# Optimization experiments

Hardware: AMD Instinct MI355X
Metric: run time of the kernel (lower is better)

Reference implementation:

```python
import jax, jax.numpy as jnp
import numpy as np

B, S, D = 8, 1024, 1024
H, KV, HD = 16, 16, 64
NDIM = 2
EPS = 1e-6


def rms_norm(x, weight=None, eps=EPS):
    var = jnp.mean(jnp.square(x), axis=-1, keepdims=True)
    out = x * jax.lax.rsqrt(var + eps)
    if weight is not None:
        out = out * weight
    return out


def rotate_half(x):
    half = x.shape[-1] // 2
    return jnp.concatenate((-x[..., half:], x[..., :half]), axis=-1)


def multidim_rope(x, cos, sin, ndim):
    # x: [B,S,H,HD]; cos,sin: [B,S,HD]; head_dim split into ndim contiguous
    # chunks of size per = 2*(HD // (2*ndim)); rotate-half applied per chunk.
    b, s, h, hd = x.shape
    per = 2 * (hd // (2 * ndim))
    xg = x.reshape(b, s, h, ndim, per)
    cg = cos.reshape(b, s, 1, ndim, per)
    sg = sin.reshape(b, s, 1, ndim, per)
    out = xg * cg + rotate_half(xg) * sg
    return out.reshape(b, s, h, hd)


def setup_inputs() -> dict:
    key = jax.random.key(0)
    ks = jax.random.split(key, 10)
    scale = 1.0 / np.sqrt(D)
    return {
        "hidden_states": jax.random.normal(ks[0], (B, S, D), jnp.float32),
        "cos": jax.random.uniform(ks[1], (B, S, HD), jnp.float32, -1.0, 1.0),
        "sin": jax.random.uniform(ks[2], (B, S, HD), jnp.float32, -1.0, 1.0),
        "position_ids": jax.random.randint(ks[3], (B, S, NDIM), 0, 32, jnp.int32),
        "wq": jax.random.normal(ks[4], (D, H * HD), jnp.float32) * scale,
        "wk": jax.random.normal(ks[5], (D, KV * HD), jnp.float32) * scale,
        "wv": jax.random.normal(ks[6], (D, KV * HD), jnp.float32) * scale,
        "wo": jax.random.normal(ks[7], (H * HD, D), jnp.float32) * scale,
        "q_norm_w": jnp.ones((HD,), jnp.float32),
        "k_norm_w": jnp.ones((HD,), jnp.float32),
    }


def reference(hidden_states, cos, sin, position_ids, wq, wk, wv, wo, q_norm_w, k_norm_w):
    b, s, _ = hidden_states.shape
    ndim = position_ids.shape[-1]

    q = (hidden_states @ wq).reshape(b, s, H, HD)
    q = rms_norm(q, q_norm_w)
    q = multidim_rope(q, cos, sin, ndim)

    k = (hidden_states @ wk).reshape(b, s, KV, HD)
    k = rms_norm(k, k_norm_w)
    k = multidim_rope(k, cos, sin, ndim)

    v = (hidden_states @ wv).reshape(b, s, KV, HD)
    v = rms_norm(v, None)  # v_norm has no weight

    # Full (non-causal) vision attention, scaling = 1.0
    scores = jnp.einsum("bqhd,bkhd->bhqk", q, k)
    probs = jax.nn.softmax(scores, axis=-1)
    attn = jnp.einsum("bhqk,bkhd->bqhd", probs, v).reshape(b, s, H * HD)

    return attn @ wo
```

## Files before the change

### kernel.cpp

```cpp
#include <hip/hip_runtime.h>
#include <hip/hip_bf16.h>

typedef __attribute__((ext_vector_type(8))) short bf16x8;
typedef __attribute__((ext_vector_type(4))) short bf16x4;
typedef __attribute__((ext_vector_type(4))) float f32x4;

struct __align__(16) V16 { unsigned long long a, b; };

__device__ __forceinline__ float bf2f(unsigned short u) {
  union { unsigned int i; float f; } c; c.i = ((unsigned int)u) << 16; return c.f;
}
__device__ __forceinline__ unsigned short f2bf(float f) {
  unsigned int u; __builtin_memcpy(&u, &f, 4);
  u += 0x7FFFu + ((u >> 16) & 1u);
  return (unsigned short)(u >> 16);
}

__device__ __forceinline__ void async16(unsigned short* lds,
                                        const unsigned short* g) {
  __builtin_amdgcn_global_load_lds(
      (const __attribute__((address_space(1))) unsigned int*)g,
      (__attribute__((address_space(3))) unsigned int*)lds, 16, 0, 0);
}

#define FP32_MAGIC 0x3F800000u

__device__ __forceinline__ void cvt_seg(
    const void* __restrict__ src, unsigned short* __restrict__ dst,
    int n4, int i, int stride, bool f32)
{
  if (f32) {
    const float* s = (const float*)src;
    for (; i < n4; i += stride) {
      float4 v = *(const float4*)(s + (size_t)i * 4);
      ushort2 lo = { f2bf(v.x), f2bf(v.y) };
      ushort2 hi = { f2bf(v.z), f2bf(v.w) };
      *(ushort2*)(dst + (size_t)i * 4)     = lo;
      *(ushort2*)(dst + (size_t)i * 4 + 2) = hi;
    }
  } else {
    const unsigned short* s = (const unsigned short*)src;
    for (; i < n4; i += stride)
      *(ushort4*)(dst + (size_t)i * 4) = *(const ushort4*)(s + (size_t)i * 4);
  }
}

__global__ __launch_bounds__(256) void cvt_bf16(
    const void* __restrict__ src, size_t srcOff,
    unsigned short* __restrict__ dst, int n4,
    const unsigned int* __restrict__ fmt)
{
  const bool f32 = (fmt[0] == FP32_MAGIC);
  const int i = blockIdx.x * blockDim.x + threadIdx.x;
  const int stride = gridDim.x * blockDim.x;
  const void* s = f32 ? (const void*)((const float*)src + srcOff)
                      : (const void*)((const unsigned short*)src + srcOff);
  cvt_seg(s, dst, n4, i, stride, f32);
}

__global__ __launch_bounds__(256) void cvt_all(
    const void* __restrict__ hid, const void* __restrict__ cosr,
    const void* __restrict__ sinr, const void* __restrict__ qnw,
    const void* __restrict__ knw,
    unsigned short* __restrict__ hb, unsigned short* __restrict__ csb,
    unsigned short* __restrict__ snb, unsigned short* __restrict__ qnb,
    unsigned short* __restrict__ knb,
    int hidden_n4, const unsigned int* __restrict__ fmt)
{
  const bool f32 = (fmt[0] == FP32_MAGIC);
  const int bx = blockIdx.x, tid = threadIdx.x;
  if (bx < 2048) {
    if (hidden_n4 > 0)
      cvt_seg(hid, hb, hidden_n4, bx * 256 + tid, 2048 * 256, f32);
  } else if (bx < 2176) {
    cvt_seg(cosr, csb, 131072, (bx - 2048) * 256 + tid, 128 * 256, f32);
  } else if (bx < 2304) {
    cvt_seg(sinr, snb, 131072, (bx - 2176) * 256 + tid, 128 * 256, f32);
  } else {
    if (tid < 16)       cvt_seg(qnw, qnb, 16, tid, 16, f32);
    else if (tid < 32)  cvt_seg(knw, knb, 16, tid - 16, 16, f32);
  }
}

__global__ __launch_bounds__(256) void cvt_t4(
    const void* __restrict__ s0, const void* __restrict__ s1,
    const void* __restrict__ s2, const void* __restrict__ s3,
    unsigned short* __restrict__ d0, unsigned short* __restrict__ d1,
    unsigned short* __restrict__ d2, unsigned short* __restrict__ d3,
    const unsigned int* __restrict__ fmt)
{
  __shared__ __align__(16) unsigned short T[64][72];
  const int z = blockIdx.z;
  const void* src = (z == 0) ? s0 : (z == 1) ? s1 : (z == 2) ? s2 : s3;
  unsigned short* dstT = (z == 0) ? d0 : (z == 1) ? d1 : (z == 2) ? d2 : d3;

  const bool f32 = (fmt[0] == FP32_MAGIC);
  const int tid = threadIdx.x;
  const int k0 = blockIdx.x * 64, n0 = blockIdx.y * 64;
  const int rl = tid >> 3, cl = (tid & 7) * 8;

#pragma unroll
  for (int p = 0; p < 2; ++p) {
    int r = rl + p * 32;
    int cs = cl ^ (r & 56);
    if (f32) {
      const float* s = (const float*)src + (size_t)(k0 + r) * 1024 + n0 + cl;
      float4 v0 = *(const float4*)s, v1 = *(const float4*)(s + 4);
      unsigned short* t = &T[r][cs];
      t[0]=f2bf(v0.x); t[1]=f2bf(v0.y); t[2]=f2bf(v0.z); t[3]=f2bf(v0.w);
      t[4]=f2bf(v1.x); t[5]=f2bf(v1.y); t[6]=f2bf(v1.z); t[7]=f2bf(v1.w);
    } else {
      *(V16*)&T[r][cs] = *(const V16*)((const unsigned short*)src +
                                        (size_t)(k0 + r) * 1024 + n0 + cl);
    }
  }
  __syncthreads();

#pragma unroll
  for (int p = 0; p < 2; ++p) {
    int u = tid + p * 256;
    int d = u >> 3, sc = (u & 7) * 8;
    unsigned short tmp[8];
#pragma unroll
    for (int i = 0; i < 8; ++i) tmp[i] = T[sc + i][d ^ sc];
    *(V16*)&dstT[(size_t)(n0 + d) * 1024 + k0 + sc] = *(V16*)tmp;
  }
}

#define TM 128
#define TN 128
#define TK 64
#define GK 1024

__global__ __launch_bounds__(256) void gemm_qkv(
    const unsigned short* __restrict__ A,
    const unsigned short* __restrict__ Bt,
    unsigned short* __restrict__ Cq,
    unsigned short* __restrict__ Ck,
    unsigned short* __restrict__ Cv,
    const unsigned short* __restrict__ cs,
    const unsigned short* __restrict__ sn,
    const unsigned short* __restrict__ qw,
    const unsigned short* __restrict__ kw,
    int M)
{
  __shared__ __align__(16) unsigned short LDSu[2 * TM * TK];
  unsigned short (*As)[TK] = (unsigned short (*)[TK])LDSu;
  unsigned short (*Bs)[TK] = (unsigned short (*)[TK])&LDSu[TM * TK];

  const int tid  = threadIdx.x;
  const int wave = tid >> 6;
  const int lane = tid & 63;
  const int quad = lane >> 4;
  const int l16  = lane & 15;
  const int bm = blockIdx.x * TM;
  const int bn = blockIdx.y * TN;
  const int wm = (wave & 1) * 64;
  const int wn = (wave >> 1) * 64;

  const f32x4 z = {0.f, 0.f, 0.f, 0.f};
  f32x4 acc[4][4];
#pragma unroll
  for (int i = 0; i < 4; ++i)
#pragma unroll
    for (int j = 0; j < 4; ++j) acc[i][j] = z;

  const int lrow = lane >> 3;
  const int gcol = ((lane & 7) ^ lrow) * 8;
  const unsigned short* aP = A  + (size_t)(bm + wave * 8 + lrow) * GK + gcol;
  const unsigned short* bP = Bt + (size_t)(bn + wave * 8 + lrow) * GK + gcol;
  const int cswz = l16 & 7;

  for (int k0 = 0; k0 < GK; k0 += TK) {
#pragma unroll
    for (int p = 0; p < 4; ++p) {
      async16(&As[p * 32 + wave * 8][0], aP + (size_t)p * 32 * GK);
      async16(&Bs[p * 32 + wave * 8][0], bP + (size_t)p * 32 * GK);
    }
    aP += TK; bP += TK;
    __syncthreads();

#pragma unroll
    for (int s = 0; s < 2; ++s) {
      const int pc = ((s * 4 + quad) ^ cswz) * 8;
      bf16x8 af[4], bfv[4];
#pragma unroll
      for (int mt = 0; mt < 4; ++mt)
        af[mt] = *(const bf16x8*)&As[wm + mt * 16 + l16][pc];
#pragma unroll
      for (int nt = 0; nt < 4; ++nt)
        bfv[nt] = *(const bf16x8*)&Bs[wn + nt * 16 + l16][pc];
#pragma unroll
      for (int mt = 0; mt < 4; ++mt)
#pragma unroll
        for (int nt = 0; nt < 4; ++nt)
          acc[mt][nt] = __builtin_amdgcn_mfma_f32_16x16x32_bf16(
              af[mt], bfv[nt], acc[mt][nt], 0, 0, 0);
    }
    __syncthreads();
  }

  const int which = bn >> 10;
  const int colbase = (bn & 1023) + wn;

  if (which == 2) {
    unsigned short* Tw = LDSu + wave * 4096;
#pragma unroll
    for (int mt = 0; mt < 4; ++mt)
#pragma unroll
      for (int r = 0; r < 4; ++r) {
        const int s = mt * 16 + quad * 4 + r;
        float x0 = acc[mt][0][r], x1 = acc[mt][1][r];
        float x2 = acc[mt][2][r], x3 = acc[mt][3][r];
        float ss = x0 * x0 + x1 * x1 + x2 * x2 + x3 * x3;
        ss += __shfl_xor(ss, 1);
        ss += __shfl_xor(ss, 2);
        ss += __shfl_xor(ss, 4);
        ss += __shfl_xor(ss, 8);
        const float inv = rsqrtf(ss * (1.f / 64.f) + 1e-6f);
        const int sw = (s >> 3) << 3;
#pragma unroll
        for (int nt = 0; nt < 4; ++nt)
          Tw[s * 64 + ((nt * 16 + l16) ^ sw)] = f2bf(acc[mt][nt][r] * inv);
      }
    __builtin_amdgcn_wave_barrier();

    const int vhead = ((bm >> 10) * 16 + (colbase >> 6)) * 64;
    const int sbase = (bm & 1023) + wm;
    const int sg = (lane & 7) * 8;
    const int dl = lane >> 3;
#pragma unroll
    for (int p = 0; p < 8; ++p) {
      const int d = p * 8 + dl;
      unsigned short tmp[8];
#pragma unroll
      for (int i = 0; i < 8; ++i)
        tmp[i] = Tw[(sg + i) * 64 + (d ^ sg)];
      *(V16*)&Cv[(size_t)(vhead + d) * 1024 + sbase + sg] = *(V16*)tmp;
    }
    return;
  }

  unsigned short* Cd = (which == 0) ? Cq : Ck;
  float wgt[4];
#pragma unroll
  for (int nt = 0; nt < 4; ++nt) {
    int d = nt * 16 + l16;
    wgt[nt] = (which == 0) ? bf2f(qw[d]) * 1.44269504f : bf2f(kw[d]);
  }

#pragma unroll
  for (int mt = 0; mt < 4; ++mt)
#pragma unroll
    for (int r = 0; r < 4; ++r) {
      const int row = bm + wm + mt * 16 + quad * 4 + r;
      float x0 = acc[mt][0][r], x1 = acc[mt][1][r];
      float x2 = acc[mt][2][r], x3 = acc[mt][3][r];
      float ss = x0 * x0 + x1 * x1 + x2 * x2 + x3 * x3;
      ss += __shfl_xor(ss, 1);
      ss += __shfl_xor(ss, 2);
      ss += __shfl_xor(ss, 4);
      ss += __shfl_xor(ss, 8);
      const float inv = rsqrtf(ss * (1.f / 64.f) + 1e-6f);
      float y[4] = { x0 * inv * wgt[0], x1 * inv * wgt[1],
                     x2 * inv * wgt[2], x3 * inv * wgt[3] };
      const unsigned short* cp = cs + (size_t)row * 64 + l16;
      const unsigned short* sp = sn + (size_t)row * 64 + l16;
#pragma unroll
      for (int nt = 0; nt < 4; ++nt) {
        float c = bf2f(cp[nt * 16]), s = bf2f(sp[nt * 16]);
        float part = (nt & 1) ? y[nt ^ 1] : -y[nt ^ 1];
        Cd[(size_t)row * 1024 + colbase + nt * 16 + l16] =
            f2bf(y[nt] * c + part * s);
      }
    }
}

__global__ __launch_bounds__(256) void gemm_bf16(
    const unsigned short* __restrict__ A,
    const unsigned short* __restrict__ Bt,
    void* __restrict__ C, size_t cOff,
    const unsigned int* __restrict__ outFmt,
    int M, int N)
{
  __shared__ __align__(16) unsigned short As[TM][TK];
  __shared__ __align__(16) unsigned short Bs[TN][TK];

  const int tid  = threadIdx.x;
  const int wave = tid >> 6;
  const int lane = tid & 63;
  const int quad = lane >> 4;
  const int l16  = lane & 15;
  const int bm = blockIdx.x * TM;
  const int bn = blockIdx.y * TN;
  const int wm = (wave & 1) * 64;
  const int wn = (wave >> 1) * 64;

  const f32x4 z = {0.f, 0.f, 0.f, 0.f};
  f32x4 acc[4][4];
#pragma unroll
  for (int i = 0; i < 4; ++i)
#pragma unroll
    for (int j = 0; j < 4; ++j) acc[i][j] = z;

  const int lrow = lane >> 3;
  const int gcol = ((lane & 7) ^ lrow) * 8;
  const unsigned short* aP = A  + (size_t)(bm + wave * 8 + lrow) * GK + gcol;
  const unsigned short* bP = Bt + (size_t)(bn + wave * 8 + lrow) * GK + gcol;
  const int cswz = l16 & 7;

  for (int k0 = 0; k0 < GK; k0 += TK) {
#pragma unroll
    for (int p = 0; p < 4; ++p) {
      async16(&As[p * 32 + wave * 8][0], aP + (size_t)p * 32 * GK);
      async16(&Bs[p * 32 + wave * 8][0], bP + (size_t)p * 32 * GK);
    }
    aP += TK; bP += TK;
    __syncthreads();

#pragma unroll
    for (int s = 0; s < 2; ++s) {
      const int pc = ((s * 4 + quad) ^ cswz) * 8;
      bf16x8 af[4], bfv[4];
#pragma unroll
      for (int mt = 0; mt < 4; ++mt)
        af[mt] = *(const bf16x8*)&As[wm + mt * 16 + l16][pc];
#pragma unroll
      for (int nt = 0; nt < 4; ++nt)
        bfv[nt] = *(const bf16x8*)&Bs[wn + nt * 16 + l16][pc];
#pragma unroll
      for (int mt = 0; mt < 4; ++mt)
#pragma unroll
        for (int nt = 0; nt < 4; ++nt)
          acc[mt][nt] = __builtin_amdgcn_mfma_f32_16x16x32_bf16(
              af[mt], bfv[nt], acc[mt][nt], 0, 0, 0);
    }
    __syncthreads();
  }

  const bool of32 = (outFmt != nullptr) && (outFmt[0] == FP32_MAGIC);
  float* Cf = (float*)C + cOff;
  unsigned short* Ch = (unsigned short*)C + cOff;

#pragma unroll
  for (int mt = 0; mt < 4; ++mt)
#pragma unroll
    for (int nt = 0; nt < 4; ++nt)
#pragma unroll
      for (int r = 0; r < 4; ++r) {
        int row = bm + wm + mt * 16 + quad * 4 + r;
        int col = bn + wn + nt * 16 + l16;
        size_t idx = (size_t)row * N + col;
        if (of32) Cf[idx] = acc[mt][nt][r];
        else      Ch[idx] = f2bf(acc[mt][nt][r]);
      }
}

__global__ __launch_bounds__(256) void attn_fused(
    const unsigned short* __restrict__ q,
    const unsigned short* __restrict__ k,
    const unsigned short* __restrict__ vt,
    unsigned short* __restrict__ o)
{
  __shared__ __align__(16) unsigned short Ks[2][64][64];
  __shared__ __align__(16) unsigned short Vs[2][64][64];

  const int tid  = threadIdx.x;
  const int wave = tid >> 6;
  const int lane = tid & 63;
  const int quad = lane >> 4;
  const int l16  = lane & 15;
  const int bh = blockIdx.y;
  const int b  = bh >> 4, h = bh & 15;
  const int qbase = blockIdx.x * 64 + wave * 16;
  const size_t bbase = (size_t)b * 1024;

  bf16x8 qf[2];
  {
    const unsigned short* qp = q + (bbase + qbase + l16) * 1024 + h * 64;
    qf[0] = *(const bf16x8*)(qp + quad * 8);
    qf[1] = *(const bf16x8*)(qp + 32 + quad * 8);
  }

  const f32x4 z = {0.f, 0.f, 0.f, 0.f};
  f32x4 of[5];
#pragma unroll
  for (int nt = 0; nt < 5; ++nt) of[nt] = z;
  float m_run = -1e30f;

  const bf16x8 onesv = { 0x3F80, 0x3F80, 0x3F80, 0x3F80,
                         0x3F80, 0x3F80, 0x3F80, 0x3F80 };

  const int lrow = lane >> 3;
  const int gcol = ((lane & 7) ^ lrow) * 8;
  const unsigned short* kP = k  + (bbase + wave * 8 + lrow) * 1024 + h * 64 + gcol;
  const unsigned short* vP = vt + ((size_t)bh * 64 + wave * 8 + lrow) * 1024 + gcol;
  const int cswz = l16 & 7;

  auto STAGE = [&](int buf, int kt) {
#pragma unroll
    for (int p = 0; p < 2; ++p) {
      async16(&Ks[buf][p * 32 + wave * 8][0], kP + ((size_t)kt * 64 + p * 32) * 1024);
      async16(&Vs[buf][p * 32 + wave * 8][0], vP + (size_t)p * 32 * 1024 + kt * 64);
    }
  };

  STAGE(0, 0);
  __syncthreads();

#pragma unroll 2
  for (int kt = 0; kt < 16; ++kt) {
    const int cur = kt & 1;
    if (kt < 15) STAGE(cur ^ 1, kt + 1);

    f32x4 sf[4];
#pragma unroll
    for (int nt = 0; nt < 4; ++nt) sf[nt] = z;
    __builtin_amdgcn_s_setprio(1);
#pragma unroll
    for (int s = 0; s < 2; ++s) {
      const int pc = ((s * 4 + quad) ^ cswz) * 8;
#pragma unroll
      for (int nt = 0; nt < 4; ++nt) {
        bf16x8 kf = *(const bf16x8*)&Ks[cur][nt * 16 + l16][pc];
        sf[nt] = __builtin_amdgcn_mfma_f32_16x16x32_bf16(kf, qf[s], sf[nt], 0, 0, 0);
      }
    }
    __builtin_amdgcn_s_setprio(0);

    float m0 = fmaxf(fmaxf(sf[0][0], sf[0][1]), fmaxf(sf[0][2], sf[0][3]));
    float m1 = fmaxf(fmaxf(sf[1][0], sf[1][1]), fmaxf(sf[1][2], sf[1][3]));
    float m2 = fmaxf(fmaxf(sf[2][0], sf[2][1]), fmaxf(sf[2][2], sf[2][3]));
    float m3 = fmaxf(fmaxf(sf[3][0], sf[3][1]), fmaxf(sf[3][2], sf[3][3]));
    float mx = fmaxf(fmaxf(m0, m1), fmaxf(m2, m3));
    mx = fmaxf(mx, __shfl_xor(mx, 16));
    mx = fmaxf(mx, __shfl_xor(mx, 32));

    if (!__all(mx - m_run <= 11.5f)) {
      float mn = fmaxf(m_run, mx);
      float alpha = __builtin_amdgcn_exp2f(m_run - mn);
      m_run = mn;
      float ar[4];
#pragma unroll
      for (int r = 0; r < 4; ++r) ar[r] = __shfl(alpha, quad * 4 + r);
#pragma unroll
      for (int nt = 0; nt < 5; ++nt)
#pragma unroll
        for (int r = 0; r < 4; ++r) of[nt][r] *= ar[r];
    }

    bf16x8 pf[2];
#pragma unroll
    for (int nt = 0; nt < 4; ++nt)
#pragma unroll
      for (int r = 0; r < 4; ++r)
        pf[nt >> 1][(nt & 1) * 4 + r] =
            (short)f2bf(__builtin_amdgcn_exp2f(sf[nt][r] - m_run));

    __builtin_amdgcn_s_setprio(1);
#pragma unroll
    for (int s = 0; s < 2; ++s) {
#pragma unroll
      for (int nt = 0; nt < 4; ++nt) {
        const unsigned short* vrow = &Vs[cur][nt * 16 + l16][0];
        const int g0  = (4 * s + (quad >> 1)) ^ cswz;
        const int off = 4 * (quad & 1);
        bf16x4 v0 = *(const bf16x4*)(vrow + g0 * 8 + off);
        bf16x4 v1 = *(const bf16x4*)(vrow + (g0 ^ 2) * 8 + off);
        bf16x8 vf = __builtin_shufflevector(v0, v1, 0, 1, 2, 3, 4, 5, 6, 7);
        of[nt] = __builtin_amdgcn_mfma_f32_16x16x32_bf16(pf[s], vf, of[nt], 0, 0, 0);
      }
      of[4] = __builtin_amdgcn_mfma_f32_16x16x32_bf16(pf[s], onesv, of[4], 0, 0, 0);
    }
    __builtin_amdgcn_s_setprio(0);

    __syncthreads();
  }

  float invl[4];
#pragma unroll
  for (int r = 0; r < 4; ++r) invl[r] = 1.f / of[4][r];
#pragma unroll
  for (int nt = 0; nt < 4; ++nt)
#pragma unroll
    for (int r = 0; r < 4; ++r) {
      int row = qbase + quad * 4 + r;
      o[(bbase + row) * 1024 + h * 64 + nt * 16 + l16] = f2bf(of[nt][r] * invl[r]);
    }
}

extern "C" void kernel_launch(void* const* d_in, const int* in_sizes, int n_in,
                              void* d_out, int out_size, void* d_ws, size_t ws_size,
                              hipStream_t stream) {
  const void* hidden = d_in[0];
  const void* cosr   = d_in[1];
  const void* sinr   = d_in[2];
  const void* wq     = d_in[4];
  const void* wk     = d_in[5];
  const void* wv     = d_in[6];
  const void* wo     = d_in[7];
  const void* qnw    = d_in[8];
  const void* knw    = d_in[9];
  const unsigned int* fmt = (const unsigned int*)qnw;

  const size_t MEG = 1024 * 1024;
  dim3 blk(256);
  unsigned short* w = (unsigned short*)d_ws;

  if (ws_size >= (size_t)60 * MEG) {
    unsigned short* hb   = w;
    unsigned short* wqT  = w + 8 * MEG;
    unsigned short* wkT  = w + 9 * MEG;
    unsigned short* wvT  = w + 10 * MEG;
    unsigned short* woT  = w + 11 * MEG;
    unsigned short* csb  = w + 12 * MEG;
    unsigned short* snb  = w + 12 * MEG + 512 * 1024;
    unsigned short* qnb  = w + 13 * MEG;
    unsigned short* knb  = w + 13 * MEG + 64;
    unsigned short* qb   = w + 14 * MEG;
    unsigned short* kb   = w + 22 * MEG;
    unsigned short* vtb  = (unsigned short*)d_out;
    unsigned short* ab   = qb;

    cvt_all<<<dim3(2305), blk, 0, stream>>>(hidden, cosr, sinr, qnw, knw,
                                            hb, csb, snb, qnb, knb,
                                            2 * (int)MEG, fmt);
    cvt_t4<<<dim3(16, 16, 4), blk, 0, stream>>>(wq, wk, wv, wo,
                                                wqT, wkT, wvT, woT, fmt);

    const int M = 8192;
    gemm_qkv<<<dim3(M / TM, 24), blk, 0, stream>>>(hb, wqT, qb, kb, vtb,
                                                   csb, snb, qnb, knb, M);
    attn_fused<<<dim3(16, 8 * 16), blk, 0, stream>>>(qb, kb, vtb, ab);
    gemm_bf16<<<dim3(M / TM, 8), blk, 0, stream>>>(ab, woT, d_out, 0, fmt,
                                                   M, 1024);
  } else {
    unsigned short* wqT  = w;
    unsigned short* wkT  = w + 1 * MEG;
    unsigned short* wvT  = w + 2 * MEG;
    unsigned short* woT  = w + 3 * MEG;
    unsigned short* csb  = w + 4 * MEG;
    unsigned short* snb  = w + 4 * MEG + 512 * 1024;
    unsigned short* qnb  = w + 5 * MEG;
    unsigned short* knb  = w + 5 * MEG + 64;
    unsigned short* hbb  = w + 6 * MEG;
    unsigned short* qb   = w + 7 * MEG;
    unsigned short* kb   = w + 8 * MEG;
    unsigned short* vtb  = w + 10 * MEG;

    cvt_t4<<<dim3(16, 16, 4), blk, 0, stream>>>(wq, wk, wv, wo,
                                                wqT, wkT, wvT, woT, fmt);
    cvt_all<<<dim3(2305), blk, 0, stream>>>(hidden, cosr, sinr, qnw, knw,
                                            nullptr, csb, snb, qnb, knb,
                                            0, fmt);

    const int Mb = 1024;
    for (int b = 0; b < 8; ++b) {
      cvt_bf16<<<dim3(512), blk, 0, stream>>>(hidden, (size_t)b * MEG, hbb,
                                              (int)(MEG / 4), fmt);
      gemm_qkv<<<dim3(Mb / TM, 24), blk, 0, stream>>>(
          hbb, wqT, qb, kb, vtb, csb + (size_t)b * 64 * 1024,
          snb + (size_t)b * 64 * 1024, qnb, knb, Mb);
      attn_fused<<<dim3(16, 16), blk, 0, stream>>>(qb, kb, vtb, qb);
      gemm_bf16<<<dim3(Mb / TM, 8), blk, 0, stream>>>(qb, woT, d_out,
                                                      (size_t)b * MEG, fmt,
                                                      Mb, 1024);
    }
  }
}
```

Baseline: 270.8 us.

## Process two query tiles per wave in attention to reuse K/V fragments

Each wave in the fused attention kernel now handles 32 query rows (two 16-row tiles) instead of 16, so each block covers 128 queries and the grid is halved. Every K and V fragment read from LDS feeds two MFMAs, which halves K/V staging traffic and LDS reads per query. In exchange, per-thread register use roughly doubles (accumulators, scores, probabilities). The rescale branch now fires if either tile needs it, and the launch bound requests 3 blocks per CU. Fewer blocks also means less parallelism for the grid.

```diff
diff --git a/kernel.cpp b/kernel.cpp
--- a/kernel.cpp
+++ b/kernel.cpp
@@ -356,7 +356,7 @@
       }
 }
 
-__global__ __launch_bounds__(256) void attn_fused(
+__global__ __launch_bounds__(256, 3) void attn_fused(
     const unsigned short* __restrict__ q,
     const unsigned short* __restrict__ k,
     const unsigned short* __restrict__ vt,
@@ -372,21 +372,23 @@
   const int l16  = lane & 15;
   const int bh = blockIdx.y;
   const int b  = bh >> 4, h = bh & 15;
-  const int qbase = blockIdx.x * 64 + wave * 16;
+  const int qbase = blockIdx.x * 128 + wave * 32;
   const size_t bbase = (size_t)b * 1024;
 
-  bf16x8 qf[2];
+  bf16x8 qfA[2], qfB[2];
   {
     const unsigned short* qp = q + (bbase + qbase + l16) * 1024 + h * 64;
-    qf[0] = *(const bf16x8*)(qp + quad * 8);
-    qf[1] = *(const bf16x8*)(qp + 32 + quad * 8);
+    qfA[0] = *(const bf16x8*)(qp + quad * 8);
+    qfA[1] = *(const bf16x8*)(qp + 32 + quad * 8);
+    qfB[0] = *(const bf16x8*)(qp + 16 * 1024 + quad * 8);
+    qfB[1] = *(const bf16x8*)(qp + 16 * 1024 + 32 + quad * 8);
   }
 
   const f32x4 z = {0.f, 0.f, 0.f, 0.f};
-  f32x4 of[5];
-#pragma unroll
-  for (int nt = 0; nt < 5; ++nt) of[nt] = z;
-  float m_run = -1e30f;
+  f32x4 ofA[5], ofB[5];
+#pragma unroll
+  for (int nt = 0; nt < 5; ++nt) { ofA[nt] = z; ofB[nt] = z; }
+  float mA = -1e30f, mB = -1e30f;
 
   const bf16x8 onesv = { 0x3F80, 0x3F80, 0x3F80, 0x3F80,
                          0x3F80, 0x3F80, 0x3F80, 0x3F80 };
@@ -413,9 +415,9 @@
     const int cur = kt & 1;
     if (kt < 15) STAGE(cur ^ 1, kt + 1);
 
-    f32x4 sf[4];
-#pragma unroll
-    for (int nt = 0; nt < 4; ++nt) sf[nt] = z;
+    f32x4 sA[4], sB[4];
+#pragma unroll
+    for (int nt = 0; nt < 4; ++nt) { sA[nt] = z; sB[nt] = z; }
     __builtin_amdgcn_s_setprio(1);
 #pragma unroll
     for (int s = 0; s < 2; ++s) {
@@ -423,39 +425,61 @@
 #pragma unroll
       for (int nt = 0; nt < 4; ++nt) {
         bf16x8 kf = *(const bf16x8*)&Ks[cur][nt * 16 + l16][pc];
-        sf[nt] = __builtin_amdgcn_mfma_f32_16x16x32_bf16(kf, qf[s], sf[nt], 0, 0, 0);
+        sA[nt] = __builtin_amdgcn_mfma_f32_16x16x32_bf16(kf, qfA[s], sA[nt], 0, 0, 0);
+        sB[nt] = __builtin_amdgcn_mfma_f32_16x16x32_bf16(kf, qfB[s], sB[nt], 0, 0, 0);
       }
     }
     __builtin_amdgcn_s_setprio(0);
 
-    float m0 = fmaxf(fmaxf(sf[0][0], sf[0][1]), fmaxf(sf[0][2], sf[0][3]));
-    float m1 = fmaxf(fmaxf(sf[1][0], sf[1][1]), fmaxf(sf[1][2], sf[1][3]));
-    float m2 = fmaxf(fmaxf(sf[2][0], sf[2][1]), fmaxf(sf[2][2], sf[2][3]));
-    float m3 = fmaxf(fmaxf(sf[3][0], sf[3][1]), fmaxf(sf[3][2], sf[3][3]));
-    float mx = fmaxf(fmaxf(m0, m1), fmaxf(m2, m3));
-    mx = fmaxf(mx, __shfl_xor(mx, 16));
-    mx = fmaxf(mx, __shfl_xor(mx, 32));
-
-    if (!__all(mx - m_run <= 11.5f)) {
-      float mn = fmaxf(m_run, mx);
-      float alpha = __builtin_amdgcn_exp2f(m_run - mn);
-      m_run = mn;
-      float ar[4];
-#pragma unroll
-      for (int r = 0; r < 4; ++r) ar[r] = __shfl(alpha, quad * 4 + r);
+    float mxA, mxB;
+    {
+      float a0 = fmaxf(fmaxf(sA[0][0], sA[0][1]), fmaxf(sA[0][2], sA[0][3]));
+      float a1 = fmaxf(fmaxf(sA[1][0], sA[1][1]), fmaxf(sA[1][2], sA[1][3]));
+      float a2 = fmaxf(fmaxf(sA[2][0], sA[2][1]), fmaxf(sA[2][2], sA[2][3]));
+      float a3 = fmaxf(fmaxf(sA[3][0], sA[3][1]), fmaxf(sA[3][2], sA[3][3]));
+      mxA = fmaxf(fmaxf(a0, a1), fmaxf(a2, a3));
+      mxA = fmaxf(mxA, __shfl_xor(mxA, 16));
+      mxA = fmaxf(mxA, __shfl_xor(mxA, 32));
+      float b0 = fmaxf(fmaxf(sB[0][0], sB[0][1]), fmaxf(sB[0][2], sB[0][3]));
+      float b1 = fmaxf(fmaxf(sB[1][0], sB[1][1]), fmaxf(sB[1][2], sB[1][3]));
+      float b2 = fmaxf(fmaxf(sB[2][0], sB[2][1]), fmaxf(sB[2][2], sB[2][3]));
+      float b3 = fmaxf(fmaxf(sB[3][0], sB[3][1]), fmaxf(sB[3][2], sB[3][3]));
+      mxB = fmaxf(fmaxf(b0, b1), fmaxf(b2, b3));
+      mxB = fmaxf(mxB, __shfl_xor(mxB, 16));
+      mxB = fmaxf(mxB, __shfl_xor(mxB, 32));
+    }
+
+    if (!__all((mxA - mA <= 11.5f) && (mxB - mB <= 11.5f))) {
+      float mnA = fmaxf(mA, mxA);
+      float mnB = fmaxf(mB, mxB);
+      float aA = __builtin_amdgcn_exp2f(mA - mnA);
+      float aB = __builtin_amdgcn_exp2f(mB - mnB);
+      mA = mnA; mB = mnB;
+      float arA[4], arB[4];
+#pragma unroll
+      for (int r = 0; r < 4; ++r) {
+        arA[r] = __shfl(aA, quad * 4 + r);
+        arB[r] = __shfl(aB, quad * 4 + r);
+      }
 #pragma unroll
       for (int nt = 0; nt < 5; ++nt)
 #pragma unroll
-        for (int r = 0; r < 4; ++r) of[nt][r] *= ar[r];
-    }
-
-    bf16x8 pf[2];
+        for (int r = 0; r < 4; ++r) {
+          ofA[nt][r] *= arA[r];
+          ofB[nt][r] *= arB[r];
+        }
+    }
+
+    bf16x8 pA[2], pB[2];
 #pragma unroll
     for (int nt = 0; nt < 4; ++nt)
 #pragma unroll
-      for (int r = 0; r < 4; ++r)
-        pf[nt >> 1][(nt & 1) * 4 + r] =
-            (short)f2bf(__builtin_amdgcn_exp2f(sf[nt][r] - m_run));
+      for (int r = 0; r < 4; ++r) {
+        pA[nt >> 1][(nt & 1) * 4 + r] =
+            (short)f2bf(__builtin_amdgcn_exp2f(sA[nt][r] - mA));
+        pB[nt >> 1][(nt & 1) * 4 + r] =
+            (short)f2bf(__builtin_amdgcn_exp2f(sB[nt][r] - mB));
+      }
 
     __builtin_amdgcn_s_setprio(1);
 #pragma unroll
@@ -468,24 +492,30 @@
         bf16x4 v0 = *(const bf16x4*)(vrow + g0 * 8 + off);
         bf16x4 v1 = *(const bf16x4*)(vrow + (g0 ^ 2) * 8 + off);
         bf16x8 vf = __builtin_shufflevector(v0, v1, 0, 1, 2, 3, 4, 5, 6, 7);
-        of[nt] = __builtin_amdgcn_mfma_f32_16x16x32_bf16(pf[s], vf, of[nt], 0, 0, 0);
+        ofA[nt] = __builtin_amdgcn_mfma_f32_16x16x32_bf16(pA[s], vf, ofA[nt], 0, 0, 0);
+        ofB[nt] = __builtin_amdgcn_mfma_f32_16x16x32_bf16(pB[s], vf, ofB[nt], 0, 0, 0);
       }
-      of[4] = __builtin_amdgcn_mfma_f32_16x16x32_bf16(pf[s], onesv, of[4], 0, 0, 0);
+      ofA[4] = __builtin_amdgcn_mfma_f32_16x16x32_bf16(pA[s], onesv, ofA[4], 0, 0, 0);
+      ofB[4] = __builtin_amdgcn_mfma_f32_16x16x32_bf16(pB[s], onesv, ofB[4], 0, 0, 0);
     }
     __builtin_amdgcn_s_setprio(0);
 
     __syncthreads();
   }
 
-  float invl[4];
-#pragma unroll
-  for (int r = 0; r < 4; ++r) invl[r] = 1.f / of[4][r];
+  float ilA[4], ilB[4];
+#pragma unroll
+  for (int r = 0; r < 4; ++r) {
+    ilA[r] = 1.f / ofA[4][r];
+    ilB[r] = 1.f / ofB[4][r];
+  }
 #pragma unroll
   for (int nt = 0; nt < 4; ++nt)
 #pragma unroll
     for (int r = 0; r < 4; ++r) {
       int row = qbase + quad * 4 + r;
-      o[(bbase + row) * 1024 + h * 64 + nt * 16 + l16] = f2bf(of[nt][r] * invl[r]);
+      o[(bbase + row) * 1024 + h * 64 + nt * 16 + l16] = f2bf(ofA[nt][r] * ilA[r]);
+      o[(bbase + row + 16) * 1024 + h * 64 + nt * 16 + l16] = f2bf(ofB[nt][r] * ilB[r]);
     }
 }
 
@@ -531,7 +561,7 @@
     const int M = 8192;
     gemm_qkv<<<dim3(M / TM, 24), blk, 0, stream>>>(hb, wqT, qb, kb, vtb,
                                                    csb, snb, qnb, knb, M);
-    attn_fused<<<dim3(16, 8 * 16), blk, 0, stream>>>(qb, kb, vtb, ab);
+    attn_fused<<<dim3(8, 8 * 16), blk, 0, stream>>>(qb, kb, vtb, ab);
     gemm_bf16<<<dim3(M / TM, 8), blk, 0, stream>>>(ab, woT, d_out, 0, fmt,
                                                    M, 1024);
   } else {
@@ -561,7 +591,7 @@
       gemm_qkv<<<dim3(Mb / TM, 24), blk, 0, stream>>>(
           hbb, wqT, qb, kb, vtb, csb + (size_t)b * 64 * 1024,
           snb + (size_t)b * 64 * 1024, qnb, knb, Mb);
-      attn_fused<<<dim3(16, 16), blk, 0, stream>>>(qb, kb, vtb, qb);
+      attn_fused<<<dim3(8, 16), blk, 0, stream>>>(qb, kb, vtb, qb);
       gemm_bf16<<<dim3(Mb / TM, 8), blk, 0, stream>>>(qb, woT, d_out,
                                                       (size_t)b * MEG, fmt,
                                                       Mb, 1024);
```

After: 260.4 us. -3.8%, faster.
